# Kernel optimization log

Hardware: AMD Instinct MI355X
Metric: run time of the kernel (lower is better)

The kernel has to match this reference:

```python
import jax, jax.numpy as jnp
import numpy as np

NUM_HEADS = 16
INPUT_DIM = 1024  # == dim == qkv_scale


def setup_inputs() -> dict:
    key = jax.random.key(0)
    k1, k2, k3 = jax.random.split(key, 3)
    x = jax.random.normal(k1, (4, 2048, INPUT_DIM), dtype=jnp.float32)
    # torch Linear(input_dim, 3*dim): y = x @ W.T + b; we store W pre-transposed as [in, out]
    W_qkv = jax.random.normal(k2, (INPUT_DIM, 3 * INPUT_DIM), dtype=jnp.float32) * (INPUT_DIM ** -0.5)
    b_qkv = jax.random.normal(k3, (3 * INPUT_DIM,), dtype=jnp.float32) * 0.01
    return {"x": x, "W_qkv": W_qkv, "b_qkv": b_qkv}


def reference(x, W_qkv, b_qkv):
    b, n, _ = x.shape
    h = NUM_HEADS
    d = INPUT_DIM // h
    scale = INPUT_DIM ** 0.5  # qkv_scale**0.5, MULTIPLIED (no softmax, no division)

    qkv = x @ W_qkv + b_qkv                      # [b, n, 3*dim]
    # rearrange 'b n (h d k) -> k b h n d': last axis splits (h, d, 3), k fastest
    qkv = qkv.reshape(b, n, h, d, 3)
    q = jnp.transpose(qkv[..., 0], (0, 2, 1, 3))  # [b, h, n, d]
    k_ = jnp.transpose(qkv[..., 1], (0, 2, 1, 3))
    v = jnp.transpose(qkv[..., 2], (0, 2, 1, 3))

    attn = jnp.einsum('bhid,bhjd->bhij', q, k_) * scale  # [b, h, n, n]
    out = jnp.einsum('bhij,bhjd->bhid', attn, v)         # [b, h, n, d]
    return out
```

## Files before the change

### kernel.cpp

```cpp
#include <hip/hip_runtime.h>
#include <stdint.h>

#define DEV __device__ __forceinline__

typedef float f32x4 __attribute__((ext_vector_type(4)));
typedef __bf16 bf16x8 __attribute__((ext_vector_type(8)));
typedef short short8 __attribute__((ext_vector_type(8)));
typedef short short4v __attribute__((ext_vector_type(4)));

DEV unsigned short f2bf(float f) {
    union { float f; unsigned u; } c; c.f = f;
    unsigned u = c.u;
    u += 0x7fffu + ((u >> 16) & 1u);
    return (unsigned short)(u >> 16);
}
DEV void async_ld16(const void* g, void* l) {
    __builtin_amdgcn_global_load_lds(
        (const __attribute__((address_space(1))) unsigned int*)g,
        (__attribute__((address_space(3))) unsigned int*)l, 16, 0, 0);
}
DEV f32x4 mfma16(bf16x8 a, bf16x8 b, f32x4 c) {
    return __builtin_amdgcn_mfma_f32_16x16x32_bf16(a, b, c, 0, 0, 0);
}

__global__ __launch_bounds__(256) void k_prep(const float* __restrict__ x,
                                              const float* __restrict__ W,
                                              unsigned short* __restrict__ xb,
                                              unsigned short* __restrict__ Wt) {
    __shared__ float T[64][65];
    const int blk = blockIdx.x, t = threadIdx.x;
    if (blk < 4096) {
        int i = blk * 256 + t;
        const float4* xp = (const float4*)x;
        float4 a = xp[i * 2], b = xp[i * 2 + 1];
        short8 o;
        o[0] = (short)f2bf(a.x); o[1] = (short)f2bf(a.y);
        o[2] = (short)f2bf(a.z); o[3] = (short)f2bf(a.w);
        o[4] = (short)f2bf(b.x); o[5] = (short)f2bf(b.y);
        o[6] = (short)f2bf(b.z); o[7] = (short)f2bf(b.w);
        *(short8*)(xb + i * 8) = o;
    } else {
        int bx = blk - 4096;
        int k0 = (bx / 48) * 64, n0 = (bx % 48) * 64;
        int rr = t >> 4, c4 = (t & 15) * 4;
        for (int i = 0; i < 4; i++) {
            int row = rr + i * 16;
            float4 v = *(const float4*)(W + (unsigned)(k0 + row) * 3072u + n0 + c4);
            T[row][c4] = v.x; T[row][c4 + 1] = v.y; T[row][c4 + 2] = v.z; T[row][c4 + 3] = v.w;
        }
        __syncthreads();
        for (int i = 0; i < 4; i++) {
            int ncol = rr + i * 16;
            int n = n0 + ncol;
            int which = n % 3;
            int oc = (n / 192) * 64 + (n % 192) / 3;
            short4v o;
            o[0] = (short)f2bf(T[c4 + 0][ncol]);
            o[1] = (short)f2bf(T[c4 + 1][ncol]);
            o[2] = (short)f2bf(T[c4 + 2][ncol]);
            o[3] = (short)f2bf(T[c4 + 3][ncol]);
            *(short4v*)(Wt + (unsigned)which * 1048576u + (unsigned)oc * 1024u + k0 + c4) = o;
        }
    }
}

__global__ __launch_bounds__(256, 2) void k_q(const unsigned short* __restrict__ Wt,
                                              const unsigned short* __restrict__ xb,
                                              const float* __restrict__ bias,
                                              unsigned short* __restrict__ Qs) {
    __shared__ __align__(16) unsigned short As[128 * 64];
    __shared__ __align__(16) unsigned short Bs[128 * 64];
    const int m0 = blockIdx.x * 128;
    const int n0 = blockIdx.y * 128;
    const int wave = threadIdx.x >> 6, lane = threadIdx.x & 63;
    const int wm = (wave & 1) * 64, wn = (wave >> 1) * 64;
    const int lan15 = lane & 15, quad = lane >> 4;
    f32x4 acc[4][4] = {};
    const int slr = wave * 32 + (lane >> 3);
    const int scs = lane & 7;

    for (int kt = 0; kt < 16; kt++) {
        __syncthreads();
        for (int i = 0; i < 4; i++) {
            int lr = slr + i * 8;
            int c = scs ^ (lr & 7);
            async_ld16(Wt + (unsigned)(m0 + lr) * 1024u + kt * 64 + c * 8,
                       (void*)(As + (wave * 32 + i * 8) * 64));
            async_ld16(xb + (unsigned)(n0 + lr) * 1024u + kt * 64 + c * 8,
                       (void*)(Bs + (wave * 32 + i * 8) * 64));
        }
        __syncthreads();
        for (int ks = 0; ks < 2; ks++) {
            bf16x8 af[4], bfr[4];
            int c0 = ks * 4 + quad;
            for (int tm = 0; tm < 4; tm++) {
                int row = wm + tm * 16 + lan15;
                af[tm] = *(const bf16x8*)(As + row * 64 + (c0 ^ (row & 7)) * 8);
            }
            for (int tn = 0; tn < 4; tn++) {
                int row = wn + tn * 16 + lan15;
                bfr[tn] = *(const bf16x8*)(Bs + row * 64 + (c0 ^ (row & 7)) * 8);
            }
            for (int tm = 0; tm < 4; tm++)
                for (int tn = 0; tn < 4; tn++)
                    acc[tm][tn] = mfma16(af[tm], bfr[tn], acc[tm][tn]);
        }
    }

    for (int tm = 0; tm < 4; tm++) {
        int oc = m0 + wm + tm * 16 + quad * 4;
        int h = oc >> 6, dd = oc & 63;
        float b0 = bias[h * 192 + (dd + 0) * 3];
        float b1 = bias[h * 192 + (dd + 1) * 3];
        float b2 = bias[h * 192 + (dd + 2) * 3];
        float b3 = bias[h * 192 + (dd + 3) * 3];
        for (int tn = 0; tn < 4; tn++) {
            int token = n0 + wn + tn * 16 + lan15;
            unsigned bb = (unsigned)(token >> 11), tl = (unsigned)(token & 2047);
            uint2 p;
            p.x = (unsigned)f2bf((acc[tm][tn][0] + b0) * 32.0f) |
                  ((unsigned)f2bf((acc[tm][tn][1] + b1) * 32.0f) << 16);
            p.y = (unsigned)f2bf((acc[tm][tn][2] + b2) * 32.0f) |
                  ((unsigned)f2bf((acc[tm][tn][3] + b3) * 32.0f) << 16);
            *(uint2*)(Qs + bb * 2097152u + tl * 1024u + oc) = p;
        }
    }
}

__global__ __launch_bounds__(256, 2) void k_kv(const unsigned short* __restrict__ xb,
                                               const unsigned short* __restrict__ Wt,
                                               const float* __restrict__ bias,
                                               unsigned short* __restrict__ K,
                                               unsigned short* __restrict__ V) {
    __shared__ __align__(16) unsigned short As[128 * 64];
    __shared__ __align__(16) unsigned short Bs[128 * 64];
    const int m0 = blockIdx.y * 128;
    const int n0 = blockIdx.x * 128;
    const int plane = 1 + (n0 >> 10);
    const int pc0 = n0 & 1023;
    const unsigned short* Wp = Wt + (unsigned)plane * 1048576u;
    const int wave = threadIdx.x >> 6, lane = threadIdx.x & 63;
    const int wm = (wave & 1) * 64, wn = (wave >> 1) * 64;
    const int lan15 = lane & 15, quad = lane >> 4;
    f32x4 acc[4][4] = {};
    const int slr = wave * 32 + (lane >> 3);
    const int scs = lane & 7;

    for (int kt = 0; kt < 16; kt++) {
        __syncthreads();
        for (int i = 0; i < 4; i++) {
            int lr = slr + i * 8;
            int c = scs ^ (lr & 7);
            async_ld16(xb + (unsigned)(m0 + lr) * 1024u + kt * 64 + c * 8,
                       (void*)(As + (wave * 32 + i * 8) * 64));
            async_ld16(Wp + (unsigned)(pc0 + lr) * 1024u + kt * 64 + c * 8,
                       (void*)(Bs + (wave * 32 + i * 8) * 64));
        }
        __syncthreads();
        for (int ks = 0; ks < 2; ks++) {
            bf16x8 af[4], bfr[4];
            int c0 = ks * 4 + quad;
            for (int tm = 0; tm < 4; tm++) {
                int row = wm + tm * 16 + lan15;
                af[tm] = *(const bf16x8*)(As + row * 64 + (c0 ^ (row & 7)) * 8);
            }
            for (int tn = 0; tn < 4; tn++) {
                int row = wn + tn * 16 + lan15;
                bfr[tn] = *(const bf16x8*)(Bs + row * 64 + (c0 ^ (row & 7)) * 8);
            }
            for (int tm = 0; tm < 4; tm++)
                for (int tn = 0; tn < 4; tn++)
                    acc[tm][tn] = mfma16(af[tm], bfr[tn], acc[tm][tn]);
        }
    }

    const int batch = m0 >> 11;
    unsigned short* dst = (plane == 1) ? K : V;
    for (int tn = 0; tn < 4; tn++) {
        int cip = pc0 + wn + tn * 16 + lan15;
        int h = cip >> 6, d = cip & 63;
        float bv = bias[h * 192 + d * 3 + plane];
        unsigned kv_base = ((unsigned)(batch * 16 + h) * 64u + (unsigned)d) * 2048u;
        for (int tm = 0; tm < 4; tm++) {
            int rbase = m0 + wm + tm * 16 + quad * 4;
            unsigned token0 = (unsigned)(rbase & 2047);
            uint2 p;
            p.x = (unsigned)f2bf(acc[tm][tn][0] + bv) |
                  ((unsigned)f2bf(acc[tm][tn][1] + bv) << 16);
            p.y = (unsigned)f2bf(acc[tm][tn][2] + bv) |
                  ((unsigned)f2bf(acc[tm][tn][3] + bv) << 16);
            *(uint2*)(dst + kv_base + token0) = p;
        }
    }
}

__global__ __launch_bounds__(256) void k_attn4(const unsigned short* __restrict__ Kt,
                                               const unsigned short* __restrict__ Vt,
                                               const unsigned short* __restrict__ Qs,
                                               float* __restrict__ out) {
    __shared__ __align__(16) unsigned short Ks[64 * 128];
    __shared__ __align__(16) unsigned short Vs[64 * 128];
    __shared__ __align__(16) unsigned short Msb[64 * 64];
    const int bh = blockIdx.x & 63, sub = blockIdx.x >> 6;
    const int b = bh >> 4, h = bh & 15;
    const int wave = threadIdx.x >> 6, lane = threadIdx.x & 63;
    const int lan15 = lane & 15, quad = lane >> 4;
    const unsigned base = (unsigned)bh * 131072u;
    const int mt0 = (wave & 1) * 2, nt0 = (wave >> 1) * 2;
    const int slr = wave * 16 + (lane >> 4), scs = lane & 15;

    f32x4 macc[2][2] = {};
    for (int j = 0; j < 16; j++) {
        __syncthreads();
        for (int i = 0; i < 4; i++) {
            int lr = slr + i * 4;
            int c = scs ^ (lr & 15);
            async_ld16(Kt + base + (unsigned)lr * 2048u + j * 128 + c * 8,
                       (void*)(Ks + (wave * 16 + i * 4) * 128));
            async_ld16(Vt + base + (unsigned)lr * 2048u + j * 128 + c * 8,
                       (void*)(Vs + (wave * 16 + i * 4) * 128));
        }
        __syncthreads();
        for (int ks2 = 0; ks2 < 4; ks2++) {
            int c0 = ks2 * 4 + quad;
            bf16x8 ak[2], bv[2];
            for (int i = 0; i < 2; i++) {
                int row = (mt0 + i) * 16 + lan15;
                ak[i] = *(const bf16x8*)(Ks + row * 128 + (c0 ^ (row & 15)) * 8);
            }
            for (int i = 0; i < 2; i++) {
                int row = (nt0 + i) * 16 + lan15;
                bv[i] = *(const bf16x8*)(Vs + row * 128 + (c0 ^ (row & 15)) * 8);
            }
            for (int i = 0; i < 2; i++)
                for (int j2 = 0; j2 < 2; j2++)
                    macc[i][j2] = mfma16(ak[i], bv[j2], macc[i][j2]);
        }
    }
    for (int i = 0; i < 2; i++)
        for (int j2 = 0; j2 < 2; j2++) {
            int d2 = (nt0 + j2) * 16 + lan15;
            int c4 = ((mt0 + i) * 4 + quad) ^ (d2 & 15);
            uint2 p;
            p.x = (unsigned)f2bf(macc[i][j2][0]) | ((unsigned)f2bf(macc[i][j2][1]) << 16);
            p.y = (unsigned)f2bf(macc[i][j2][2]) | ((unsigned)f2bf(macc[i][j2][3]) << 16);
            *(uint2*)(Msb + d2 * 64 + c4 * 4) = p;
        }
    __syncthreads();

    const int t0 = sub * 256 + wave * 64;
    f32x4 oacc[4][4] = {};
#pragma unroll
    for (int ks = 0; ks < 2; ks++) {
        bf16x8 af[4], bfr[4];
        for (int mt = 0; mt < 4; mt++) {
            int tok = t0 + mt * 16 + lan15;
            af[mt] = *(const bf16x8*)(Qs + (unsigned)b * 2097152u + (unsigned)tok * 1024u +
                                      h * 64 + ks * 32 + quad * 8);
        }
        for (int nt = 0; nt < 4; nt++) {
            int d2 = nt * 16 + lan15;
            int cA = ks * 8 + quad * 2;
            uint2 u0 = *(const uint2*)(Msb + d2 * 64 + ((cA) ^ (d2 & 15)) * 4);
            uint2 u1 = *(const uint2*)(Msb + d2 * 64 + ((cA + 1) ^ (d2 & 15)) * 4);
            union { uint4 u; bf16x8 v; } cv;
            cv.u.x = u0.x; cv.u.y = u0.y; cv.u.z = u1.x; cv.u.w = u1.y;
            bfr[nt] = cv.v;
        }
        for (int mt = 0; mt < 4; mt++)
            for (int nt = 0; nt < 4; nt++)
                oacc[mt][nt] = mfma16(af[mt], bfr[nt], oacc[mt][nt]);
    }
    for (int mt = 0; mt < 4; mt++)
        for (int nt = 0; nt < 4; nt++)
            for (int r = 0; r < 4; r++)
                out[base + (unsigned)(t0 + mt * 16 + quad * 4 + r) * 64u + nt * 16 + lan15] =
                    oacc[mt][nt][r];
}

extern "C" void kernel_launch(void* const* d_in, const int* in_sizes, int n_in,
                              void* d_out, int out_size, void* d_ws, size_t ws_size,
                              hipStream_t stream) {
    const float* x = (const float*)d_in[0];
    const float* W = (const float*)d_in[1];
    const float* b = (const float*)d_in[2];
    float* out = (float*)d_out;

    unsigned short* xb = (unsigned short*)d_ws;
    unsigned short* Wt = xb + 8388608;
    unsigned short* Qs = Wt + 3145728;
    unsigned short* Kt = Qs + 8388608;
    unsigned short* Vt = Kt + 8388608;

    k_prep<<<4864, 256, 0, stream>>>(x, W, xb, Wt);
    k_q<<<dim3(8, 64), 256, 0, stream>>>(Wt, xb, b, Qs);
    k_kv<<<dim3(16, 64), 256, 0, stream>>>(xb, Wt, b, Kt, Vt);
    k_attn4<<<512, 256, 0, stream>>>(Kt, Vt, Qs, out);
}
```

Baseline: 175.8 us.

## Fuse Q and KV projection GEMMs into one triple-buffered 256x128 tile kernel

New measurement: 190.3 us. 8.2% more time.

```diff
diff --git a/kernel.cpp b/kernel.cpp
--- a/kernel.cpp
+++ b/kernel.cpp
@@ -64,132 +64,143 @@
     }
 }
 
-__global__ __launch_bounds__(256, 2) void k_q(const unsigned short* __restrict__ Wt,
-                                              const unsigned short* __restrict__ xb,
-                                              const float* __restrict__ bias,
-                                              unsigned short* __restrict__ Qs) {
-    __shared__ __align__(16) unsigned short As[128 * 64];
-    __shared__ __align__(16) unsigned short Bs[128 * 64];
-    const int m0 = blockIdx.x * 128;
-    const int n0 = blockIdx.y * 128;
-    const int wave = threadIdx.x >> 6, lane = threadIdx.x & 63;
-    const int wm = (wave & 1) * 64, wn = (wave >> 1) * 64;
+#define BARRIER() asm volatile("s_barrier" ::: "memory")
+#define WAITV(n) do { asm volatile("s_waitcnt vmcnt(" #n ")" ::: "memory"); \
+                      __builtin_amdgcn_sched_barrier(0); } while (0)
+
+__global__ __launch_bounds__(512, 2) void k_qkv(const unsigned short* __restrict__ xb,
+                                                const unsigned short* __restrict__ Wt,
+                                                const float* __restrict__ bias,
+                                                unsigned short* __restrict__ Qs,
+                                                unsigned short* __restrict__ K,
+                                                unsigned short* __restrict__ V) {
+    __shared__ __align__(16) unsigned short As[3][256 * 64];
+    __shared__ __align__(16) unsigned short Bs[3][128 * 64];
+
+    const int o = blockIdx.x + 24 * blockIdx.y;
+    const int w = (o & 7) * 96 + (o >> 3);
+    const int mt = w / 24, nt = w % 24;
+    const int m0 = mt * 256;
+    const int plane = nt >> 3;
+    const int pc0 = (nt & 7) * 128;
+    const unsigned short* Xp = xb + (unsigned)m0 * 1024u;
+    const unsigned short* Wp = Wt + (unsigned)plane * 1048576u + (unsigned)pc0 * 1024u;
+
+    const int t = threadIdx.x;
+    const int wave = t >> 6, lane = t & 63;
     const int lan15 = lane & 15, quad = lane >> 4;
+    const int srow = t >> 3;
+    const int schunk = t & 7;
+
+    const bool swp = (plane == 0);
+    const int ga = swp ? (wave & 1) : (wave >> 1);
+    const int gb = swp ? (wave >> 1) : (wave & 1);
+
     f32x4 acc[4][4] = {};
-    const int slr = wave * 32 + (lane >> 3);
-    const int scs = lane & 7;
+
+#define STAGE(kt, b) do {                                                     \
+        const int kk_ = (kt) * 64;                                            \
+        _Pragma("unroll")                                                     \
+        for (int i_ = 0; i_ < 4; i_++) {                                      \
+            int r_ = i_ * 64 + srow;                                          \
+            int c_ = schunk ^ (r_ & 7);                                       \
+            async_ld16(Xp + (unsigned)r_ * 1024u + kk_ + c_ * 8,              \
+                       (void*)(As[b] + (i_ * 64 + wave * 8) * 64));           \
+        }                                                                     \
+        _Pragma("unroll")                                                     \
+        for (int i_ = 0; i_ < 2; i_++) {                                      \
+            int r_ = i_ * 64 + srow;                                          \
+            int c_ = schunk ^ (r_ & 7);                                       \
+            async_ld16(Wp + (unsigned)r_ * 1024u + kk_ + c_ * 8,              \
+                       (void*)(Bs[b] + (i_ * 64 + wave * 8) * 64));           \
+        }                                                                     \
+    } while (0)
+
+    STAGE(0, 0);
+    STAGE(1, 1);
 
     for (int kt = 0; kt < 16; kt++) {
-        __syncthreads();
-        for (int i = 0; i < 4; i++) {
-            int lr = slr + i * 8;
-            int c = scs ^ (lr & 7);
-            async_ld16(Wt + (unsigned)(m0 + lr) * 1024u + kt * 64 + c * 8,
-                       (void*)(As + (wave * 32 + i * 8) * 64));
-            async_ld16(xb + (unsigned)(n0 + lr) * 1024u + kt * 64 + c * 8,
-                       (void*)(Bs + (wave * 32 + i * 8) * 64));
-        }
-        __syncthreads();
+        const int buf = kt % 3;
+        if (kt + 2 < 16) {
+            STAGE(kt + 2, (kt + 2) % 3);
+            WAITV(12);
+        } else if (kt + 1 < 16) {
+            WAITV(6);
+        } else {
+            WAITV(0);
+        }
+        BARRIER();
+
+        const unsigned short* Ab = (swp ? Bs[buf] : As[buf]) + ga * 64 * 64;
+        const unsigned short* Bb = (swp ? As[buf] : Bs[buf]) + gb * 64 * 64;
+#pragma unroll
         for (int ks = 0; ks < 2; ks++) {
+            const int c0 = ks * 4 + quad;
             bf16x8 af[4], bfr[4];
-            int c0 = ks * 4 + quad;
+#pragma unroll
             for (int tm = 0; tm < 4; tm++) {
-                int row = wm + tm * 16 + lan15;
-                af[tm] = *(const bf16x8*)(As + row * 64 + (c0 ^ (row & 7)) * 8);
-            }
+                int row = tm * 16 + lan15;
+                af[tm] = *(const bf16x8*)(Ab + row * 64 + (c0 ^ (row & 7)) * 8);
+            }
+#pragma unroll
             for (int tn = 0; tn < 4; tn++) {
-                int row = wn + tn * 16 + lan15;
-                bfr[tn] = *(const bf16x8*)(Bs + row * 64 + (c0 ^ (row & 7)) * 8);
-            }
+                int row = tn * 16 + lan15;
+                bfr[tn] = *(const bf16x8*)(Bb + row * 64 + (c0 ^ (row & 7)) * 8);
+            }
+            __builtin_amdgcn_s_setprio(1);
+#pragma unroll
             for (int tm = 0; tm < 4; tm++)
+#pragma unroll
                 for (int tn = 0; tn < 4; tn++)
                     acc[tm][tn] = mfma16(af[tm], bfr[tn], acc[tm][tn]);
-        }
-    }
-
-    for (int tm = 0; tm < 4; tm++) {
-        int oc = m0 + wm + tm * 16 + quad * 4;
-        int h = oc >> 6, dd = oc & 63;
-        float b0 = bias[h * 192 + (dd + 0) * 3];
-        float b1 = bias[h * 192 + (dd + 1) * 3];
-        float b2 = bias[h * 192 + (dd + 2) * 3];
-        float b3 = bias[h * 192 + (dd + 3) * 3];
+            __builtin_amdgcn_s_setprio(0);
+        }
+        BARRIER();
+    }
+#undef STAGE
+
+    if (plane == 0) {
+        const int cg = (wave & 1) * 64, tg = (wave >> 1) * 64;
+#pragma unroll
+        for (int tm = 0; tm < 4; tm++) {
+            int c4 = pc0 + cg + tm * 16 + quad * 4;
+            int h = c4 >> 6, dd = c4 & 63;
+            float b0 = bias[h * 192 + (dd + 0) * 3];
+            float b1 = bias[h * 192 + (dd + 1) * 3];
+            float b2 = bias[h * 192 + (dd + 2) * 3];
+            float b3 = bias[h * 192 + (dd + 3) * 3];
+#pragma unroll
+            for (int tn = 0; tn < 4; tn++) {
+                int token = m0 + tg + tn * 16 + lan15;
+                unsigned bb = (unsigned)(token >> 11), tl = (unsigned)(token & 2047);
+                uint2 p;
+                p.x = (unsigned)f2bf((acc[tm][tn][0] + b0) * 32.0f) |
+                      ((unsigned)f2bf((acc[tm][tn][1] + b1) * 32.0f) << 16);
+                p.y = (unsigned)f2bf((acc[tm][tn][2] + b2) * 32.0f) |
+                      ((unsigned)f2bf((acc[tm][tn][3] + b3) * 32.0f) << 16);
+                *(uint2*)(Qs + bb * 2097152u + tl * 1024u + c4) = p;
+            }
+        }
+    } else {
+        unsigned short* dst = (plane == 1) ? K : V;
+        const int tg = (wave >> 1) * 64, cg = (wave & 1) * 64;
+        const int batch = m0 >> 11;
+#pragma unroll
         for (int tn = 0; tn < 4; tn++) {
-            int token = n0 + wn + tn * 16 + lan15;
-            unsigned bb = (unsigned)(token >> 11), tl = (unsigned)(token & 2047);
-            uint2 p;
-            p.x = (unsigned)f2bf((acc[tm][tn][0] + b0) * 32.0f) |
-                  ((unsigned)f2bf((acc[tm][tn][1] + b1) * 32.0f) << 16);
-            p.y = (unsigned)f2bf((acc[tm][tn][2] + b2) * 32.0f) |
-                  ((unsigned)f2bf((acc[tm][tn][3] + b3) * 32.0f) << 16);
-            *(uint2*)(Qs + bb * 2097152u + tl * 1024u + oc) = p;
-        }
-    }
-}
-
-__global__ __launch_bounds__(256, 2) void k_kv(const unsigned short* __restrict__ xb,
-                                               const unsigned short* __restrict__ Wt,
-                                               const float* __restrict__ bias,
-                                               unsigned short* __restrict__ K,
-                                               unsigned short* __restrict__ V) {
-    __shared__ __align__(16) unsigned short As[128 * 64];
-    __shared__ __align__(16) unsigned short Bs[128 * 64];
-    const int m0 = blockIdx.y * 128;
-    const int n0 = blockIdx.x * 128;
-    const int plane = 1 + (n0 >> 10);
-    const int pc0 = n0 & 1023;
-    const unsigned short* Wp = Wt + (unsigned)plane * 1048576u;
-    const int wave = threadIdx.x >> 6, lane = threadIdx.x & 63;
-    const int wm = (wave & 1) * 64, wn = (wave >> 1) * 64;
-    const int lan15 = lane & 15, quad = lane >> 4;
-    f32x4 acc[4][4] = {};
-    const int slr = wave * 32 + (lane >> 3);
-    const int scs = lane & 7;
-
-    for (int kt = 0; kt < 16; kt++) {
-        __syncthreads();
-        for (int i = 0; i < 4; i++) {
-            int lr = slr + i * 8;
-            int c = scs ^ (lr & 7);
-            async_ld16(xb + (unsigned)(m0 + lr) * 1024u + kt * 64 + c * 8,
-                       (void*)(As + (wave * 32 + i * 8) * 64));
-            async_ld16(Wp + (unsigned)(pc0 + lr) * 1024u + kt * 64 + c * 8,
-                       (void*)(Bs + (wave * 32 + i * 8) * 64));
-        }
-        __syncthreads();
-        for (int ks = 0; ks < 2; ks++) {
-            bf16x8 af[4], bfr[4];
-            int c0 = ks * 4 + quad;
+            int cip = pc0 + cg + tn * 16 + lan15;
+            int h = cip >> 6, d = cip & 63;
+            float bv = bias[h * 192 + d * 3 + plane];
+            unsigned kv_base = ((unsigned)(batch * 16 + h) * 64u + (unsigned)d) * 2048u;
+#pragma unroll
             for (int tm = 0; tm < 4; tm++) {
-                int row = wm + tm * 16 + lan15;
-                af[tm] = *(const bf16x8*)(As + row * 64 + (c0 ^ (row & 7)) * 8);
-            }
-            for (int tn = 0; tn < 4; tn++) {
-                int row = wn + tn * 16 + lan15;
-                bfr[tn] = *(const bf16x8*)(Bs + row * 64 + (c0 ^ (row & 7)) * 8);
-            }
-            for (int tm = 0; tm < 4; tm++)
-                for (int tn = 0; tn < 4; tn++)
-                    acc[tm][tn] = mfma16(af[tm], bfr[tn], acc[tm][tn]);
-        }
-    }
-
-    const int batch = m0 >> 11;
-    unsigned short* dst = (plane == 1) ? K : V;
-    for (int tn = 0; tn < 4; tn++) {
-        int cip = pc0 + wn + tn * 16 + lan15;
-        int h = cip >> 6, d = cip & 63;
-        float bv = bias[h * 192 + d * 3 + plane];
-        unsigned kv_base = ((unsigned)(batch * 16 + h) * 64u + (unsigned)d) * 2048u;
-        for (int tm = 0; tm < 4; tm++) {
-            int rbase = m0 + wm + tm * 16 + quad * 4;
-            unsigned token0 = (unsigned)(rbase & 2047);
-            uint2 p;
-            p.x = (unsigned)f2bf(acc[tm][tn][0] + bv) |
-                  ((unsigned)f2bf(acc[tm][tn][1] + bv) << 16);
-            p.y = (unsigned)f2bf(acc[tm][tn][2] + bv) |
-                  ((unsigned)f2bf(acc[tm][tn][3] + bv) << 16);
-            *(uint2*)(dst + kv_base + token0) = p;
+                unsigned token0 = (unsigned)((m0 + tg + tm * 16 + quad * 4) & 2047);
+                uint2 p;
+                p.x = (unsigned)f2bf(acc[tm][tn][0] + bv) |
+                      ((unsigned)f2bf(acc[tm][tn][1] + bv) << 16);
+                p.y = (unsigned)f2bf(acc[tm][tn][2] + bv) |
+                      ((unsigned)f2bf(acc[tm][tn][3] + bv) << 16);
+                *(uint2*)(dst + kv_base + token0) = p;
+            }
         }
     }
 }
@@ -293,7 +304,6 @@
     unsigned short* Vt = Kt + 8388608;
 
     k_prep<<<4864, 256, 0, stream>>>(x, W, xb, Wt);
-    k_q<<<dim3(8, 64), 256, 0, stream>>>(Wt, xb, b, Qs);
-    k_kv<<<dim3(16, 64), 256, 0, stream>>>(xb, Wt, b, Kt, Vt);
+    k_qkv<<<dim3(24, 32), 512, 0, stream>>>(xb, Wt, b, Qs, Kt, Vt);
     k_attn4<<<512, 256, 0, stream>>>(Kt, Vt, Qs, out);
 }
```

## Split attention into chunked KᵀV partial kernel and Q·M output kernel

Applied to the files above, without the earlier changes.

New measurement: 182.5 us. 3.8% more time.

```diff
diff --git a/kernel.cpp b/kernel.cpp
--- a/kernel.cpp
+++ b/kernel.cpp
@@ -194,88 +194,115 @@
     }
 }
 
-__global__ __launch_bounds__(256) void k_attn4(const unsigned short* __restrict__ Kt,
-                                               const unsigned short* __restrict__ Vt,
-                                               const unsigned short* __restrict__ Qs,
-                                               float* __restrict__ out) {
+__global__ __launch_bounds__(256) void k_m(const unsigned short* __restrict__ Kt,
+                                           const unsigned short* __restrict__ Vt,
+                                           float* __restrict__ Mp) {
     __shared__ __align__(16) unsigned short Ks[64 * 128];
     __shared__ __align__(16) unsigned short Vs[64 * 128];
+    const int bh = blockIdx.x & 63, chunk = blockIdx.x >> 6;
+    const int wave = threadIdx.x >> 6, lane = threadIdx.x & 63;
+    const int lan15 = lane & 15, quad = lane >> 4;
+    const unsigned base = (unsigned)bh * 131072u;
+    const int mt0 = (wave & 1) * 2, nt0 = (wave >> 1) * 2;
+    const int slr = wave * 16 + (lane >> 4), scs = lane & 15;
+
+    f32x4 macc[2][2] = {};
+    for (int j = chunk * 4; j < chunk * 4 + 4; j++) {
+        __syncthreads();
+        for (int i = 0; i < 4; i++) {
+            int lr = slr + i * 4;
+            int c = scs ^ (lr & 15);
+            async_ld16(Kt + base + (unsigned)lr * 2048u + j * 128 + c * 8,
+                       (void*)(Ks + (wave * 16 + i * 4) * 128));
+            async_ld16(Vt + base + (unsigned)lr * 2048u + j * 128 + c * 8,
+                       (void*)(Vs + (wave * 16 + i * 4) * 128));
+        }
+        __syncthreads();
+        for (int ks2 = 0; ks2 < 4; ks2++) {
+            int c0 = ks2 * 4 + quad;
+            bf16x8 ak[2], bv[2];
+            for (int i = 0; i < 2; i++) {
+                int row = (mt0 + i) * 16 + lan15;
+                ak[i] = *(const bf16x8*)(Ks + row * 128 + (c0 ^ (row & 15)) * 8);
+            }
+            for (int i = 0; i < 2; i++) {
+                int row = (nt0 + i) * 16 + lan15;
+                bv[i] = *(const bf16x8*)(Vs + row * 128 + (c0 ^ (row & 15)) * 8);
+            }
+            for (int i = 0; i < 2; i++)
+                for (int j2 = 0; j2 < 2; j2++)
+                    macc[i][j2] = mfma16(ak[i], bv[j2], macc[i][j2]);
+        }
+    }
+    for (int i = 0; i < 2; i++)
+        for (int j2 = 0; j2 < 2; j2++) {
+            int d2 = (nt0 + j2) * 16 + lan15;
+            int d1b = (mt0 + i) * 16 + quad * 4;
+            *(f32x4*)(Mp + (((unsigned)(bh * 4 + chunk) * 64u + (unsigned)d2) * 64u + d1b)) =
+                macc[i][j2];
+        }
+}
+
+__global__ __launch_bounds__(256) void k_out(const float* __restrict__ Mp,
+                                             const unsigned short* __restrict__ Qs,
+                                             float* __restrict__ out) {
     __shared__ __align__(16) unsigned short Msb[64 * 64];
     const int bh = blockIdx.x & 63, sub = blockIdx.x >> 6;
     const int b = bh >> 4, h = bh & 15;
     const int wave = threadIdx.x >> 6, lane = threadIdx.x & 63;
     const int lan15 = lane & 15, quad = lane >> 4;
     const unsigned base = (unsigned)bh * 131072u;
-    const int mt0 = (wave & 1) * 2, nt0 = (wave >> 1) * 2;
-    const int slr = wave * 16 + (lane >> 4), scs = lane & 15;
-
-    f32x4 macc[2][2] = {};
-    for (int j = 0; j < 16; j++) {
-        __syncthreads();
-        for (int i = 0; i < 4; i++) {
-            int lr = slr + i * 4;
-            int c = scs ^ (lr & 15);
-            async_ld16(Kt + base + (unsigned)lr * 2048u + j * 128 + c * 8,
-                       (void*)(Ks + (wave * 16 + i * 4) * 128));
-            async_ld16(Vt + base + (unsigned)lr * 2048u + j * 128 + c * 8,
-                       (void*)(Vs + (wave * 16 + i * 4) * 128));
-        }
-        __syncthreads();
-        for (int ks2 = 0; ks2 < 4; ks2++) {
-            int c0 = ks2 * 4 + quad;
-            bf16x8 ak[2], bv[2];
-            for (int i = 0; i < 2; i++) {
-                int row = (mt0 + i) * 16 + lan15;
-                ak[i] = *(const bf16x8*)(Ks + row * 128 + (c0 ^ (row & 15)) * 8);
-            }
-            for (int i = 0; i < 2; i++) {
-                int row = (nt0 + i) * 16 + lan15;
-                bv[i] = *(const bf16x8*)(Vs + row * 128 + (c0 ^ (row & 15)) * 8);
-            }
-            for (int i = 0; i < 2; i++)
-                for (int j2 = 0; j2 < 2; j2++)
-                    macc[i][j2] = mfma16(ak[i], bv[j2], macc[i][j2]);
-        }
-    }
-    for (int i = 0; i < 2; i++)
-        for (int j2 = 0; j2 < 2; j2++) {
-            int d2 = (nt0 + j2) * 16 + lan15;
-            int c4 = ((mt0 + i) * 4 + quad) ^ (d2 & 15);
+
+    {
+        const int t = threadIdx.x;
+        const int d2 = t >> 2, d1b = (t & 3) * 16;
+        const float* mp0 = Mp + (((unsigned)(bh * 4) * 64u + (unsigned)d2) * 64u + d1b);
+#pragma unroll
+        for (int jj = 0; jj < 4; jj++) {
+            float4 s = *(const float4*)(mp0 + jj * 4);
+#pragma unroll
+            for (int c = 1; c < 4; c++) {
+                float4 v = *(const float4*)(mp0 + (unsigned)c * 4096u + jj * 4);
+                s.x += v.x; s.y += v.y; s.z += v.z; s.w += v.w;
+            }
+            int c4 = (t & 3) * 4 + jj;
             uint2 p;
-            p.x = (unsigned)f2bf(macc[i][j2][0]) | ((unsigned)f2bf(macc[i][j2][1]) << 16);
-            p.y = (unsigned)f2bf(macc[i][j2][2]) | ((unsigned)f2bf(macc[i][j2][3]) << 16);
-            *(uint2*)(Msb + d2 * 64 + c4 * 4) = p;
-        }
+            p.x = (unsigned)f2bf(s.x) | ((unsigned)f2bf(s.y) << 16);
+            p.y = (unsigned)f2bf(s.z) | ((unsigned)f2bf(s.w) << 16);
+            *(uint2*)(Msb + d2 * 64 + (c4 ^ (d2 & 15)) * 4) = p;
+        }
+    }
     __syncthreads();
 
     const int t0 = sub * 256 + wave * 64;
     f32x4 oacc[4][4] = {};
 #pragma unroll
     for (int ks = 0; ks < 2; ks++) {
-        bf16x8 af[4], bfr[4];
-        for (int mt = 0; mt < 4; mt++) {
-            int tok = t0 + mt * 16 + lan15;
-            af[mt] = *(const bf16x8*)(Qs + (unsigned)b * 2097152u + (unsigned)tok * 1024u +
-                                      h * 64 + ks * 32 + quad * 8);
-        }
-        for (int nt = 0; nt < 4; nt++) {
-            int d2 = nt * 16 + lan15;
+        bf16x8 mf[4], qf[4];
+        for (int tm = 0; tm < 4; tm++) {
+            int d2 = tm * 16 + lan15;
             int cA = ks * 8 + quad * 2;
             uint2 u0 = *(const uint2*)(Msb + d2 * 64 + ((cA) ^ (d2 & 15)) * 4);
             uint2 u1 = *(const uint2*)(Msb + d2 * 64 + ((cA + 1) ^ (d2 & 15)) * 4);
             union { uint4 u; bf16x8 v; } cv;
             cv.u.x = u0.x; cv.u.y = u0.y; cv.u.z = u1.x; cv.u.w = u1.y;
-            bfr[nt] = cv.v;
-        }
-        for (int mt = 0; mt < 4; mt++)
-            for (int nt = 0; nt < 4; nt++)
-                oacc[mt][nt] = mfma16(af[mt], bfr[nt], oacc[mt][nt]);
-    }
-    for (int mt = 0; mt < 4; mt++)
-        for (int nt = 0; nt < 4; nt++)
-            for (int r = 0; r < 4; r++)
-                out[base + (unsigned)(t0 + mt * 16 + quad * 4 + r) * 64u + nt * 16 + lan15] =
-                    oacc[mt][nt][r];
+            mf[tm] = cv.v;
+        }
+        for (int tn = 0; tn < 4; tn++) {
+            int tok = t0 + tn * 16 + lan15;
+            qf[tn] = *(const bf16x8*)(Qs + (unsigned)b * 2097152u + (unsigned)tok * 1024u +
+                                      h * 64 + ks * 32 + quad * 8);
+        }
+        for (int tm = 0; tm < 4; tm++)
+            for (int tn = 0; tn < 4; tn++)
+                oacc[tm][tn] = mfma16(mf[tm], qf[tn], oacc[tm][tn]);
+    }
+    for (int tm = 0; tm < 4; tm++)
+        for (int tn = 0; tn < 4; tn++) {
+            int tok = t0 + tn * 16 + lan15;
+            int d2b = tm * 16 + quad * 4;
+            *(f32x4*)(out + base + (unsigned)tok * 64u + d2b) = oacc[tm][tn];
+        }
 }
 
 extern "C" void kernel_launch(void* const* d_in, const int* in_sizes, int n_in,
@@ -291,9 +318,11 @@
     unsigned short* Qs = Wt + 3145728;
     unsigned short* Kt = Qs + 8388608;
     unsigned short* Vt = Kt + 8388608;
+    float* Mp = (float*)xb;
 
     k_prep<<<4864, 256, 0, stream>>>(x, W, xb, Wt);
     k_q<<<dim3(8, 64), 256, 0, stream>>>(Wt, xb, b, Qs);
     k_kv<<<dim3(16, 64), 256, 0, stream>>>(xb, Wt, b, Kt, Vt);
-    k_attn4<<<512, 256, 0, stream>>>(Kt, Vt, Qs, out);
-}
+    k_m<<<256, 256, 0, stream>>>(Kt, Vt, Mp);
+    k_out<<<512, 256, 0, stream>>>(Mp, Qs, out);
+}
```

## Double-buffer K/V staging in attention and vectorize output stores

Applied to the files above, without the earlier changes.

New measurement: 184.5 us. 4.9% more time.

```diff
diff --git a/kernel.cpp b/kernel.cpp
--- a/kernel.cpp
+++ b/kernel.cpp
@@ -22,6 +22,10 @@
 DEV f32x4 mfma16(bf16x8 a, bf16x8 b, f32x4 c) {
     return __builtin_amdgcn_mfma_f32_16x16x32_bf16(a, b, c, 0, 0, 0);
 }
+
+#define BARRIER() asm volatile("s_barrier" ::: "memory")
+#define WAITV(n) do { asm volatile("s_waitcnt vmcnt(" #n ")" ::: "memory"); \
+                      __builtin_amdgcn_sched_barrier(0); } while (0)
 
 __global__ __launch_bounds__(256) void k_prep(const float* __restrict__ x,
                                               const float* __restrict__ W,
@@ -30,15 +34,17 @@
     __shared__ float T[64][65];
     const int blk = blockIdx.x, t = threadIdx.x;
     if (blk < 4096) {
-        int i = blk * 256 + t;
+        const unsigned i0 = (unsigned)blk * 512u + (unsigned)t;
         const float4* xp = (const float4*)x;
-        float4 a = xp[i * 2], b = xp[i * 2 + 1];
-        short8 o;
-        o[0] = (short)f2bf(a.x); o[1] = (short)f2bf(a.y);
-        o[2] = (short)f2bf(a.z); o[3] = (short)f2bf(a.w);
-        o[4] = (short)f2bf(b.x); o[5] = (short)f2bf(b.y);
-        o[6] = (short)f2bf(b.z); o[7] = (short)f2bf(b.w);
-        *(short8*)(xb + i * 8) = o;
+#pragma unroll
+        for (int half = 0; half < 2; half++) {
+            unsigned i = i0 + (unsigned)half * 256u;
+            float4 a = xp[i];
+            short4v o;
+            o[0] = (short)f2bf(a.x); o[1] = (short)f2bf(a.y);
+            o[2] = (short)f2bf(a.z); o[3] = (short)f2bf(a.w);
+            *(short4v*)(xb + i * 4u) = o;
+        }
     } else {
         int bx = blk - 4096;
         int k0 = (bx / 48) * 64, n0 = (bx % 48) * 64;
@@ -198,8 +204,8 @@
                                                const unsigned short* __restrict__ Vt,
                                                const unsigned short* __restrict__ Qs,
                                                float* __restrict__ out) {
-    __shared__ __align__(16) unsigned short Ks[64 * 128];
-    __shared__ __align__(16) unsigned short Vs[64 * 128];
+    __shared__ __align__(16) unsigned short Ks[2][64 * 128];
+    __shared__ __align__(16) unsigned short Vs[2][64 * 128];
     __shared__ __align__(16) unsigned short Msb[64 * 64];
     const int bh = blockIdx.x & 63, sub = blockIdx.x >> 6;
     const int b = bh >> 4, h = bh & 15;
@@ -209,34 +215,44 @@
     const int mt0 = (wave & 1) * 2, nt0 = (wave >> 1) * 2;
     const int slr = wave * 16 + (lane >> 4), scs = lane & 15;
 
+#define STAGE_J(j, bf) do {                                                   \
+        _Pragma("unroll")                                                     \
+        for (int i_ = 0; i_ < 4; i_++) {                                      \
+            int lr_ = slr + i_ * 4;                                           \
+            int c_ = scs ^ (lr_ & 15);                                        \
+            async_ld16(Kt + base + (unsigned)lr_ * 2048u + (j) * 128 + c_ * 8,\
+                       (void*)(Ks[bf] + (wave * 16 + i_ * 4) * 128));         \
+            async_ld16(Vt + base + (unsigned)lr_ * 2048u + (j) * 128 + c_ * 8,\
+                       (void*)(Vs[bf] + (wave * 16 + i_ * 4) * 128));         \
+        }                                                                     \
+    } while (0)
+
     f32x4 macc[2][2] = {};
+    STAGE_J(0, 0);
     for (int j = 0; j < 16; j++) {
-        __syncthreads();
-        for (int i = 0; i < 4; i++) {
-            int lr = slr + i * 4;
-            int c = scs ^ (lr & 15);
-            async_ld16(Kt + base + (unsigned)lr * 2048u + j * 128 + c * 8,
-                       (void*)(Ks + (wave * 16 + i * 4) * 128));
-            async_ld16(Vt + base + (unsigned)lr * 2048u + j * 128 + c * 8,
-                       (void*)(Vs + (wave * 16 + i * 4) * 128));
-        }
-        __syncthreads();
+        const int bf = j & 1;
+        if (j < 15) { STAGE_J(j + 1, bf ^ 1); WAITV(8); }
+        else        { WAITV(0); }
+        BARRIER();
         for (int ks2 = 0; ks2 < 4; ks2++) {
             int c0 = ks2 * 4 + quad;
             bf16x8 ak[2], bv[2];
             for (int i = 0; i < 2; i++) {
                 int row = (mt0 + i) * 16 + lan15;
-                ak[i] = *(const bf16x8*)(Ks + row * 128 + (c0 ^ (row & 15)) * 8);
+                ak[i] = *(const bf16x8*)(Ks[bf] + row * 128 + (c0 ^ (row & 15)) * 8);
             }
             for (int i = 0; i < 2; i++) {
                 int row = (nt0 + i) * 16 + lan15;
-                bv[i] = *(const bf16x8*)(Vs + row * 128 + (c0 ^ (row & 15)) * 8);
+                bv[i] = *(const bf16x8*)(Vs[bf] + row * 128 + (c0 ^ (row & 15)) * 8);
             }
             for (int i = 0; i < 2; i++)
                 for (int j2 = 0; j2 < 2; j2++)
                     macc[i][j2] = mfma16(ak[i], bv[j2], macc[i][j2]);
         }
-    }
+        BARRIER();
+    }
+#undef STAGE_J
+
     for (int i = 0; i < 2; i++)
         for (int j2 = 0; j2 < 2; j2++) {
             int d2 = (nt0 + j2) * 16 + lan15;
@@ -252,30 +268,31 @@
     f32x4 oacc[4][4] = {};
 #pragma unroll
     for (int ks = 0; ks < 2; ks++) {
-        bf16x8 af[4], bfr[4];
-        for (int mt = 0; mt < 4; mt++) {
-            int tok = t0 + mt * 16 + lan15;
-            af[mt] = *(const bf16x8*)(Qs + (unsigned)b * 2097152u + (unsigned)tok * 1024u +
-                                      h * 64 + ks * 32 + quad * 8);
-        }
-        for (int nt = 0; nt < 4; nt++) {
-            int d2 = nt * 16 + lan15;
+        bf16x8 mf[4], qf[4];
+        for (int tm = 0; tm < 4; tm++) {
+            int d2 = tm * 16 + lan15;
             int cA = ks * 8 + quad * 2;
             uint2 u0 = *(const uint2*)(Msb + d2 * 64 + ((cA) ^ (d2 & 15)) * 4);
             uint2 u1 = *(const uint2*)(Msb + d2 * 64 + ((cA + 1) ^ (d2 & 15)) * 4);
             union { uint4 u; bf16x8 v; } cv;
             cv.u.x = u0.x; cv.u.y = u0.y; cv.u.z = u1.x; cv.u.w = u1.y;
-            bfr[nt] = cv.v;
-        }
-        for (int mt = 0; mt < 4; mt++)
-            for (int nt = 0; nt < 4; nt++)
-                oacc[mt][nt] = mfma16(af[mt], bfr[nt], oacc[mt][nt]);
-    }
-    for (int mt = 0; mt < 4; mt++)
-        for (int nt = 0; nt < 4; nt++)
-            for (int r = 0; r < 4; r++)
-                out[base + (unsigned)(t0 + mt * 16 + quad * 4 + r) * 64u + nt * 16 + lan15] =
-                    oacc[mt][nt][r];
+            mf[tm] = cv.v;
+        }
+        for (int tn = 0; tn < 4; tn++) {
+            int tok = t0 + tn * 16 + lan15;
+            qf[tn] = *(const bf16x8*)(Qs + (unsigned)b * 2097152u + (unsigned)tok * 1024u +
+                                      h * 64 + ks * 32 + quad * 8);
+        }
+        for (int tm = 0; tm < 4; tm++)
+            for (int tn = 0; tn < 4; tn++)
+                oacc[tm][tn] = mfma16(mf[tm], qf[tn], oacc[tm][tn]);
+    }
+    for (int tm = 0; tm < 4; tm++)
+        for (int tn = 0; tn < 4; tn++) {
+            int tok = t0 + tn * 16 + lan15;
+            int d2b = tm * 16 + quad * 4;
+            *(f32x4*)(out + base + (unsigned)tok * 64u + d2b) = oacc[tm][tn];
+        }
 }
 
 extern "C" void kernel_launch(void* const* d_in, const int* in_sizes, int n_in,
```
